# Performance work log

Hardware: AMD Instinct MI355X
Metric: run time of the kernel (lower is better)

The kernel has to match this reference:

```python
import jax, jax.numpy as jnp
import numpy as np

LOC_SIZE, CID_SIZE, UID_SIZE, TIM_SIZE = 10000, 300, 1000, 48
LOC_EMB, CID_EMB, UID_EMB, TIM_EMB = 256, 64, 64, 32
HID, ENC_HID = 500, 250            # hidden_size, history_hidden_size
SEQ, TGT = 2048, 256
INPUT = LOC_EMB + TIM_EMB + CID_EMB  # 352


def setup_inputs() -> dict:
    key = jax.random.key(0)
    ks = jax.random.split(key, 32)
    n = lambda i, shape, s=0.05: (jax.random.normal(ks[i], shape, dtype=jnp.float32) * s)
    d = {}
    d["loc"] = jax.random.randint(ks[0], (SEQ, 1), 0, LOC_SIZE)
    d["tim"] = jax.random.randint(ks[1], (SEQ, 1), 0, TIM_SIZE)
    d["cid"] = jax.random.randint(ks[2], (SEQ, 1), 0, CID_SIZE)
    d["uid"] = jax.random.randint(ks[3], (1,), 0, UID_SIZE)
    d["target"] = jax.random.randint(ks[4], (TGT, 1), 0, LOC_SIZE)
    d["target_len"] = TGT
    d["time_sim_matrix"] = jax.random.uniform(ks[5], (TIM_SIZE, TIM_SIZE), dtype=jnp.float32)
    # keep distances away from 0 since the model computes 1/dist
    d["poi_distance_matrix"] = jax.random.uniform(ks[6], (LOC_SIZE, LOC_SIZE), dtype=jnp.float32, minval=0.1, maxval=2.0)
    d["poi_cid_tim"] = jax.random.uniform(ks[7], (TIM_SIZE, CID_SIZE), dtype=jnp.float32)
    # embedding tables (emb_loc/emb_cid are pretrained+frozen in the original)
    d["weight"] = n(8, (LOC_SIZE, LOC_EMB))
    d["weight_cid"] = n(9, (CID_SIZE, CID_EMB))
    d["emb_uid_w"] = n(10, (UID_SIZE, UID_EMB))
    d["emb_tim_w"] = n(11, (TIM_SIZE, TIM_EMB))
    # bidirectional encoder LSTM (hidden 250), gate order i,f,g,o like torch
    d["enc_Wih_f"] = n(12, (4 * ENC_HID, INPUT))
    d["enc_Whh_f"] = n(13, (4 * ENC_HID, ENC_HID))
    d["enc_b_f"] = jnp.zeros((4 * ENC_HID,), jnp.float32)
    d["enc_Wih_b"] = n(14, (4 * ENC_HID, INPUT))
    d["enc_Whh_b"] = n(15, (4 * ENC_HID, ENC_HID))
    d["enc_b_b"] = jnp.zeros((4 * ENC_HID,), jnp.float32)
    # decoder LSTM (hidden 500)
    d["dec_Wih"] = n(16, (4 * HID, INPUT))
    d["dec_Whh"] = n(17, (4 * HID, HID))
    d["dec_b"] = jnp.zeros((4 * HID,), jnp.float32)
    # linear layers
    d["fc_user_w"] = n(18, (HID, UID_EMB))
    d["fc_user_b"] = jnp.zeros((HID,), jnp.float32)
    d["fc_final_w"] = n(19, (LOC_SIZE, 3 * HID))
    d["fc_final_b"] = jnp.zeros((LOC_SIZE,), jnp.float32)
    d["fc_final2_w"] = n(20, (HID, 3 * HID))
    d["fc_final2_b"] = jnp.zeros((HID,), jnp.float32)
    return d


def _lstm(x, Wih, Whh, b, H):
    """Single-layer LSTM, batch=1. x: [T, D] -> hs: [T, H]."""
    h0 = jnp.zeros((H,), x.dtype)
    c0 = jnp.zeros((H,), x.dtype)

    def step(carry, xt):
        h, c = carry
        z = Wih @ xt + Whh @ h + b
        i, f, g, o = jnp.split(z, 4)
        c = jax.nn.sigmoid(f) * c + jax.nn.sigmoid(i) * jnp.tanh(g)
        h = jax.nn.sigmoid(o) * jnp.tanh(c)
        return (h, c), h

    _, hs = jax.lax.scan(step, (h0, c0), x)
    return hs


def _table_attn(history, current, table, invert=False, causal=False):
    """Vectorized replacement for the nested-loop lookup attention.
    energies[i, j] = table[current[i], history[j]] (or its reciprocal),
    upper triangle left at 0 for the self-attn variants (as in the original),
    then softmax over the full row (torch F.softmax default dim=1 on 2D)."""
    e = table[current[:, None], history[None, :]]
    if invert:
        e = 1.0 / e
    if causal:
        nn_ = e.shape[0]
        e = jnp.where(jnp.tril(jnp.ones((nn_, nn_), bool)), e, jnp.zeros((), e.dtype))
    return jax.nn.softmax(e, axis=-1)


def reference(loc, tim, cid, uid, target, target_len,
              time_sim_matrix, poi_distance_matrix, poi_cid_tim,
              weight, weight_cid, emb_uid_w, emb_tim_w,
              enc_Wih_f, enc_Whh_f, enc_b_f, enc_Wih_b, enc_Whh_b, enc_b_b,
              dec_Wih, dec_Whh, dec_b,
              fc_user_w, fc_user_b, fc_final_w, fc_final_b, fc_final2_w, fc_final2_b):
    T = int(target_len)
    loc_f, tim_f, cid_f = loc[:, 0], tim[:, 0], cid[:, 0]

    # cross attention: current window attends to history via lookup tables
    attn_cid_time = _table_attn(cid_f[:-T], tim_f[-T:], poi_cid_tim)
    attn_loc = _table_attn(loc_f[:-T], loc_f[-T:], poi_distance_matrix, invert=True)
    attn_time = _table_attn(tim_f[:-T], tim_f[-T:], time_sim_matrix)
    # self attention on the current window (lower-triangular fill)
    self_cid_time = _table_attn(cid_f[-T:], tim_f[-T:], poi_cid_tim, causal=True)
    self_loc = _table_attn(loc_f[-T:], loc_f[-T:], poi_distance_matrix, invert=True, causal=True)
    self_time = _table_attn(tim_f[-T:], tim_f[-T:], time_sim_matrix, causal=True)

    # embeddings (dropout is identity in eval)
    x = jnp.concatenate([weight[loc_f], emb_tim_w[tim_f], weight_cid[cid_f]], axis=1)  # [SEQ, INPUT]
    hist_x, tgt_x = x[:-T], x[-T:]

    # bidirectional encoder over history
    hf = _lstm(hist_x, enc_Wih_f, enc_Whh_f, enc_b_f, ENC_HID)
    hb = _lstm(hist_x[::-1], enc_Wih_b, enc_Whh_b, enc_b_b, ENC_HID)[::-1]
    hidden_history = jnp.concatenate([hf, hb], axis=1)  # [SEQ-T, 2*ENC_HID=500]

    # decoder over current window
    hidden_state = _lstm(tgt_x, dec_Wih, dec_Whh, dec_b, HID)  # [T, 500]

    target_emb = weight[target[:, 0]]  # [T, LOC_EMB]

    uid_emb = emb_uid_w[uid] @ fc_user_w.T + fc_user_b  # [1, 500]
    user_attn = jax.nn.softmax(uid_emb @ hidden_history.T, axis=-1)  # [1, hist]
    context_user = user_attn @ hidden_history  # [1, 500]

    context = (attn_loc + attn_time + attn_cid_time) @ hidden_history  # [T, 500]
    hidden_state = (self_loc + self_time + self_cid_time) @ hidden_state  # [T, 500]

    hidden_state_all = hidden_state + uid_emb  # broadcast of repeat
    out = jnp.concatenate([hidden_state_all, context,
                           jnp.broadcast_to(context_user, (T, HID))], axis=1)  # [T, 1500]
    y = out @ fc_final_w.T + fc_final_b    # [T, LOC_SIZE]
    y1 = out @ fc_final2_w.T + fc_final2_b  # [T, HID]
    score = jax.nn.log_softmax(y, axis=-1)
    return score, y1, target_emb
```

## Files before the change

### kernel.cpp

```cpp
#include <hip/hip_runtime.h>
#include <stdint.h>

#define HIST 1792
#define TGT 256
#define SEQ 2048
#define INPUT 352
#define EHID 250
#define HID 500

typedef _Float16 h2_t __attribute__((ext_vector_type(2)));

static __device__ __forceinline__ float fdot2(uint32_t a, uint32_t b, float c) {
  return __builtin_amdgcn_fdot2(__builtin_bit_cast(h2_t, a),
                                __builtin_bit_cast(h2_t, b), c, false);
}
static __device__ __forceinline__ uint32_t packh2(float lo, float hi) {
  h2_t h; h[0] = (_Float16)lo; h[1] = (_Float16)hi;
  return __builtin_bit_cast(uint32_t, h);
}
static __device__ __forceinline__ uint4 packq(const float* p) {
  uint4 r;
  r.x = packh2(p[0], p[1]); r.y = packh2(p[2], p[3]);
  r.z = packh2(p[4], p[5]); r.w = packh2(p[6], p[7]);
  return r;
}
static __device__ __forceinline__ float dotq(uint4 w, uint4 h, float acc) {
  acc = fdot2(w.x, h.x, acc); acc = fdot2(w.y, h.y, acc);
  acc = fdot2(w.z, h.z, acc); acc = fdot2(w.w, h.w, acc);
  return acc;
}
static __device__ __forceinline__ float sigf(float x) {
  x = fminf(fmaxf(x, -30.f), 30.f);
  return 1.f / (1.f + __expf(-x));
}
static __device__ __forceinline__ float tanh_f(float x) {
  x = fminf(fmaxf(x, -15.f), 15.f);
  float e = __expf(2.f * x);
  return (e - 1.f) / (e + 1.f);
}
static __device__ __forceinline__ void spin_flag(volatile int* f) {
  while (__hip_atomic_load(f, __ATOMIC_ACQUIRE, __HIP_MEMORY_SCOPE_AGENT) == 0)
    __builtin_amdgcn_s_sleep(2);
}
static __device__ __forceinline__ void spin_cnt(volatile int* f, int target) {
  while (__hip_atomic_load(f, __ATOMIC_ACQUIRE, __HIP_MEMORY_SCOPE_AGENT) < target)
    __builtin_amdgcn_s_sleep(2);
}
#define AW(dst, src) asm("v_accvgpr_write_b32 %0, %1" : "=a"(dst) : "v"(src))
#define AR(dst, src) asm("v_accvgpr_read_b32 %0, %1" : "=v"(dst) : "a"(src))
#define ARQ(dst, arr, base) do { AR(dst.x, arr[(base)+0]); AR(dst.y, arr[(base)+1]); AR(dst.z, arr[(base)+2]); AR(dst.w, arr[(base)+3]); } while(0)

__global__ void k_gemm_t16(const float* __restrict__ A, int lda,
                           const float* __restrict__ W, int ldw,
                           const float* __restrict__ bias,
                           float* __restrict__ C, int ldc,
                           int M, int N, int K, int revA) {
  __shared__ uint32_t AsP[8][65];
  __shared__ uint32_t WsP[8][65];
  const int bn = blockIdx.x * 64, bm = blockIdx.y * 64;
  const int tid = threadIdx.x;
  const int tx = tid & 15, ty = tid >> 4;
  float acc[4][4] = {};
  for (int k0 = 0; k0 < K; k0 += 16) {
    for (int i = tid; i < 512; i += 256) {
      int m = i & 63, kk = i >> 6;
      int gm = bm + m, gk = k0 + 2 * kk;
      float v0 = 0.f, v1 = 0.f;
      if (gm < M) {
        int am = revA ? (M - 1 - gm) : gm;
        if (gk < K)     v0 = A[(size_t)am * lda + gk];
        if (gk + 1 < K) v1 = A[(size_t)am * lda + gk + 1];
      }
      AsP[kk][m] = packh2(v0, v1);
    }
    for (int i = tid; i < 512; i += 256) {
      int n = i & 63, kk = i >> 6;
      int gn = bn + n, gk = k0 + 2 * kk;
      float v0 = 0.f, v1 = 0.f;
      if (gn < N) {
        if (gk < K)     v0 = W[(size_t)gn * ldw + gk];
        if (gk + 1 < K) v1 = W[(size_t)gn * ldw + gk + 1];
      }
      WsP[kk][n] = packh2(v0, v1);
    }
    __syncthreads();
#pragma unroll
    for (int kk = 0; kk < 8; kk++) {
      uint32_t a0 = AsP[kk][ty * 4 + 0], a1 = AsP[kk][ty * 4 + 1], a2 = AsP[kk][ty * 4 + 2], a3 = AsP[kk][ty * 4 + 3];
      uint32_t b0 = WsP[kk][tx * 4 + 0], b1 = WsP[kk][tx * 4 + 1], b2 = WsP[kk][tx * 4 + 2], b3 = WsP[kk][tx * 4 + 3];
      acc[0][0] = fdot2(a0, b0, acc[0][0]); acc[0][1] = fdot2(a0, b1, acc[0][1]);
      acc[0][2] = fdot2(a0, b2, acc[0][2]); acc[0][3] = fdot2(a0, b3, acc[0][3]);
      acc[1][0] = fdot2(a1, b0, acc[1][0]); acc[1][1] = fdot2(a1, b1, acc[1][1]);
      acc[1][2] = fdot2(a1, b2, acc[1][2]); acc[1][3] = fdot2(a1, b3, acc[1][3]);
      acc[2][0] = fdot2(a2, b0, acc[2][0]); acc[2][1] = fdot2(a2, b1, acc[2][1]);
      acc[2][2] = fdot2(a2, b2, acc[2][2]); acc[2][3] = fdot2(a2, b3, acc[2][3]);
      acc[3][0] = fdot2(a3, b0, acc[3][0]); acc[3][1] = fdot2(a3, b1, acc[3][1]);
      acc[3][2] = fdot2(a3, b2, acc[3][2]); acc[3][3] = fdot2(a3, b3, acc[3][3]);
    }
    __syncthreads();
  }
  for (int i = 0; i < 4; i++) {
    int gm = bm + ty * 4 + i; if (gm >= M) continue;
    for (int j = 0; j < 4; j++) {
      int gn = bn + tx * 4 + j; if (gn >= N) continue;
      C[(size_t)gm * ldc + gn] = acc[i][j] + (bias ? bias[gn] : 0.f);
    }
  }
}

static __device__ void gemm_tile_emb(const int* __restrict__ loc, const int* __restrict__ tim,
                                     const int* __restrict__ cid,
                                     const float* __restrict__ weight,
                                     const float* __restrict__ emb_tim_w,
                                     const float* __restrict__ weight_cid,
                                     int rowoff,
                                     const float* __restrict__ W,
                                     const float* __restrict__ bias,
                                     float* __restrict__ C, int ldc,
                                     int M, int N, int bm, int bn, int revA,
                                     int tid, uint32_t* AsP, uint32_t* WsP) {
  const int tx = tid & 15, ty = (tid & 255) >> 4;
  float acc[4][4] = {};
  for (int k0 = 0; k0 < INPUT; k0 += 16) {
    {
      int m = tid & 63, kk = tid >> 6;
      int gm = bm + m, gk = k0 + 2 * kk;
      float v0 = 0.f, v1 = 0.f;
      if (gm < M) {
        int am = (revA ? (M - 1 - gm) : gm) + rowoff;
        if (gk < 256) {
          const float* wp = weight + (size_t)loc[am] * 256 + gk;
          v0 = wp[0]; v1 = wp[1];
        } else if (gk < 288) {
          const float* wp = emb_tim_w + tim[am] * 32 + (gk - 256);
          v0 = wp[0]; v1 = wp[1];
        } else {
          const float* wp = weight_cid + cid[am] * 64 + (gk - 288);
          v0 = wp[0]; v1 = wp[1];
        }
      }
      AsP[kk * 65 + m] = packh2(v0, v1);
      int gn = bn + m;
      float w0 = 0.f, w1 = 0.f;
      if (gn < N) {
        const float* wp = W + (size_t)gn * INPUT + gk;
        w0 = wp[0]; w1 = wp[1];
      }
      WsP[kk * 65 + m] = packh2(w0, w1);
    }
    __syncthreads();
    if (tid < 256) {
#pragma unroll
      for (int kk = 0; kk < 8; kk++) {
        uint32_t a0 = AsP[kk * 65 + ty * 4 + 0], a1 = AsP[kk * 65 + ty * 4 + 1];
        uint32_t a2 = AsP[kk * 65 + ty * 4 + 2], a3 = AsP[kk * 65 + ty * 4 + 3];
        uint32_t b0 = WsP[kk * 65 + tx * 4 + 0], b1 = WsP[kk * 65 + tx * 4 + 1];
        uint32_t b2 = WsP[kk * 65 + tx * 4 + 2], b3 = WsP[kk * 65 + tx * 4 + 3];
        acc[0][0] = fdot2(a0, b0, acc[0][0]); acc[0][1] = fdot2(a0, b1, acc[0][1]);
        acc[0][2] = fdot2(a0, b2, acc[0][2]); acc[0][3] = fdot2(a0, b3, acc[0][3]);
        acc[1][0] = fdot2(a1, b0, acc[1][0]); acc[1][1] = fdot2(a1, b1, acc[1][1]);
        acc[1][2] = fdot2(a1, b2, acc[1][2]); acc[1][3] = fdot2(a1, b3, acc[1][3]);
        acc[2][0] = fdot2(a2, b0, acc[2][0]); acc[2][1] = fdot2(a2, b1, acc[2][1]);
        acc[2][2] = fdot2(a2, b2, acc[2][2]); acc[2][3] = fdot2(a2, b3, acc[2][3]);
        acc[3][0] = fdot2(a3, b0, acc[3][0]); acc[3][1] = fdot2(a3, b1, acc[3][1]);
        acc[3][2] = fdot2(a3, b2, acc[3][2]); acc[3][3] = fdot2(a3, b3, acc[3][3]);
      }
    }
    __syncthreads();
  }
  if (tid < 256) {
    for (int i = 0; i < 4; i++) {
      int gm = bm + ty * 4 + i; if (gm >= M) continue;
      for (int j = 0; j < 4; j++) {
        int gn = bn + tx * 4 + j; if (gn >= N) continue;
        C[(size_t)gm * ldc + gn] = acc[i][j] + bias[gn];
      }
    }
  }
}

static __device__ void nn_tile_fused(const float* __restrict__ A, int lda,
                                     const float* __restrict__ B, int ldb,
                                     const float* __restrict__ addvec,
                                     float* __restrict__ C, int ldc,
                                     int M, int N, int K, int bm, int bn,
                                     int tid, uint32_t* AsP, uint32_t* BsP) {
  const int tx = tid & 15, ty = (tid & 255) >> 4;
  float acc[4][4] = {};
  for (int k0 = 0; k0 < K; k0 += 16) {
    {
      int m = tid & 63, kk = tid >> 6;
      int gm = bm + m, gk = k0 + 2 * kk;
      float v0 = 0.f, v1 = 0.f;
      if (gm < M) {
        if (gk < K)     v0 = A[(size_t)gm * lda + gk];
        if (gk + 1 < K) v1 = A[(size_t)gm * lda + gk + 1];
      }
      AsP[kk * 65 + m] = packh2(v0, v1);
      int gn = bn + m;
      float w0 = 0.f, w1 = 0.f;
      if (gn < N) {
        if (gk < K)     w0 = B[(size_t)gk * ldb + gn];
        if (gk + 1 < K) w1 = B[(size_t)(gk + 1) * ldb + gn];
      }
      BsP[kk * 65 + m] = packh2(w0, w1);
    }
    __syncthreads();
    if (tid < 256) {
#pragma unroll
      for (int kk = 0; kk < 8; kk++) {
        uint32_t a0 = AsP[kk * 65 + ty * 4 + 0], a1 = AsP[kk * 65 + ty * 4 + 1];
        uint32_t a2 = AsP[kk * 65 + ty * 4 + 2], a3 = AsP[kk * 65 + ty * 4 + 3];
        uint32_t b0 = BsP[kk * 65 + tx * 4 + 0], b1 = BsP[kk * 65 + tx * 4 + 1];
        uint32_t b2 = BsP[kk * 65 + tx * 4 + 2], b3 = BsP[kk * 65 + tx * 4 + 3];
        acc[0][0] = fdot2(a0, b0, acc[0][0]); acc[0][1] = fdot2(a0, b1, acc[0][1]);
        acc[0][2] = fdot2(a0, b2, acc[0][2]); acc[0][3] = fdot2(a0, b3, acc[0][3]);
        acc[1][0] = fdot2(a1, b0, acc[1][0]); acc[1][1] = fdot2(a1, b1, acc[1][1]);
        acc[1][2] = fdot2(a1, b2, acc[1][2]); acc[1][3] = fdot2(a1, b3, acc[1][3]);
        acc[2][0] = fdot2(a2, b0, acc[2][0]); acc[2][1] = fdot2(a2, b1, acc[2][1]);
        acc[2][2] = fdot2(a2, b2, acc[2][2]); acc[2][3] = fdot2(a2, b3, acc[2][3]);
        acc[3][0] = fdot2(a3, b0, acc[3][0]); acc[3][1] = fdot2(a3, b1, acc[3][1]);
        acc[3][2] = fdot2(a3, b2, acc[3][2]); acc[3][3] = fdot2(a3, b3, acc[3][3]);
      }
    }
    __syncthreads();
  }
  if (tid < 256) {
    for (int i = 0; i < 4; i++) {
      int gm = bm + ty * 4 + i; if (gm >= M) continue;
      for (int j = 0; j < 4; j++) {
        int gn = bn + tx * 4 + j; if (gn >= N) continue;
        C[(size_t)gm * ldc + gn] = acc[i][j] + (addvec ? addvec[gn] : 0.f);
      }
    }
  }
}

#define WQL 12
#define WBYTES (WQL * 512 * 16)
__launch_bounds__(512)
__global__ void k_lstm(float* __restrict__ A_f, float* __restrict__ A_b,
                       float* __restrict__ A_d,
                       const float* __restrict__ Wih_f, const float* __restrict__ b_f,
                       const float* __restrict__ Wih_b, const float* __restrict__ b_b,
                       const float* __restrict__ Wih_d, const float* __restrict__ b_d,
                       const float* __restrict__ Whh_f, const float* __restrict__ Whh_b,
                       const float* __restrict__ Whh_d,
                       float* __restrict__ hh, float* __restrict__ hdec,
                       float* zpub, uint32_t* hpub, int* flag_z, int* flag_h, int* cnt,
                       const int* __restrict__ loc, const int* __restrict__ tim,
                       const int* __restrict__ cid, const int* __restrict__ target,
                       const float* __restrict__ weight, const float* __restrict__ emb_tim_w,
                       const float* __restrict__ weight_cid,
                       const float* __restrict__ ts, const float* __restrict__ pd,
                       const float* __restrict__ pct,
                       float* __restrict__ S1, float* __restrict__ S2,
                       const int* __restrict__ uid, const float* __restrict__ emb_uid_w,
                       const float* __restrict__ fc_user_w, const float* __restrict__ fc_user_b,
                       float* __restrict__ uid_emb, float* __restrict__ te) {
  const int b = blockIdx.x;
  const int tid = threadIdx.x;
  __shared__ __align__(16) unsigned char smem[WBYTES + 2048 + 4096];
  uint4* wl = (uint4*)smem;
  uint4* hbuf = (uint4*)(smem + WBYTES);
  float* zbuf = (float*)(smem + WBYTES + 2048);

  if (b < 6 && tid < 128) hbuf[tid] = make_uint4(0, 0, 0, 0);

  if (b < 2) {
    float* A = (b == 0) ? A_f : A_b;
    const float* Whh = (b == 0) ? Whh_f : Whh_b;
    int* mycnt = cnt + b * 32;
    const bool act = tid < 500;
    uint4 wv0[10], wv1[10];
    uint32_t wa[128];
    if (act) {
      const float* wr0 = Whh + (size_t)tid * EHID;
      const float* wr1 = Whh + (size_t)(tid + 500) * EHID;
#pragma unroll
      for (int q = 0; q < 6; q++) {
        float t0[8], t1[8];
#pragma unroll
        for (int cc = 0; cc < 8; cc++) {
          int col = 208 + 8 * q + cc;
          t0[cc] = (col < EHID) ? wr0[col] : 0.f;
          t1[cc] = (col < EHID) ? wr1[col] : 0.f;
        }
        wl[(q * 2 + 0) * 512 + tid] = packq(t0);
        wl[(q * 2 + 1) * 512 + tid] = packq(t1);
      }
#pragma unroll
      for (int k = 0; k < 16; k++) {
        uint4 p0 = packq(wr0 + 8 * (10 + k));
        uint4 p1 = packq(wr1 + 8 * (10 + k));
        AW(wa[k * 4 + 0], p0.x); AW(wa[k * 4 + 1], p0.y);
        AW(wa[k * 4 + 2], p0.z); AW(wa[k * 4 + 3], p0.w);
        AW(wa[64 + k * 4 + 0], p1.x); AW(wa[64 + k * 4 + 1], p1.y);
        AW(wa[64 + k * 4 + 2], p1.z); AW(wa[64 + k * 4 + 3], p1.w);
      }
#pragma unroll
      for (int q = 0; q < 10; q++) { wv0[q] = packq(wr0 + 8 * q); wv1[q] = packq(wr1 + 8 * q); }
    }
    if (tid == 0) spin_cnt(&mycnt[0], 16);
    __syncthreads();
    float c = 0.f;
    float aA = act ? A[tid] : 0.f;
    float aB = act ? A[500 + tid] : 0.f;
    __syncthreads();
    for (int t = 0; t < HIST; t++) {
      const uint4* hb = hbuf + (t & 1) * 32;
      int tn = (t + 1 < HIST) ? t + 1 : t;
      if ((tn & 63) == 0 && tn > t) {
        if (tid == 0) spin_cnt(&mycnt[tn >> 6], 16);
        __syncthreads();
      }
      if (act) {
        float z0 = aA, z1 = aB, y0 = 0.f, y1 = 0.f;
        aA = A[tn * 1000 + tid];
        aB = A[tn * 1000 + 500 + tid];
#pragma unroll
        for (int q = 0; q < 10; q++) {
          uint4 hq = hb[q];
          z0 = dotq(wv0[q], hq, z0);
          z1 = dotq(wv1[q], hq, z1);
        }
#pragma unroll
        for (int k = 0; k < 16; k++) {
          uint4 hq = hb[10 + k];
          uint4 u0, u1;
          ARQ(u0, wa, k * 4);
          ARQ(u1, wa, 64 + k * 4);
          y0 = dotq(u0, hq, y0);
          y1 = dotq(u1, hq, y1);
        }
#pragma unroll
        for (int q = 0; q < 6; q++) {
          uint4 hq = hb[26 + q];
          z0 = dotq(wl[(q * 2 + 0) * 512 + tid], hq, z0);
          z1 = dotq(wl[(q * 2 + 1) * 512 + tid], hq, z1);
        }
        zbuf[tid] = z0 + y0;
        zbuf[500 + tid] = z1 + y1;
      }
      __syncthreads();
      float hval = 0.f;
      if (tid < EHID) {
        float zi = zbuf[tid], zf = zbuf[250 + tid], zg = zbuf[500 + tid], zo = zbuf[750 + tid];
        c = sigf(zf) * c + sigf(zi) * tanh_f(zg);
        hval = sigf(zo) * tanh_f(c);
        if (b == 0) hh[(size_t)t * HID + tid] = hval;
        else        hh[(size_t)(HIST - 1 - t) * HID + EHID + tid] = hval;
      }
      float hother = __shfl_xor(hval, 1);
      uint32_t* hw = (uint32_t*)(hbuf + ((t + 1) & 1) * 32);
      if (tid < EHID && !(tid & 1)) hw[tid >> 1] = packh2(hval, hother);
      __syncthreads();
    }
  } else if (b < 6) {
    const int gi = b - 2;
    const int j = tid;
    const bool act = (j < 500);
    int* dcnt = cnt + 64;
    uint4 wv[20];
    uint32_t wa[128];
    if (act) {
      const float* wr = Whh_d + (size_t)(gi * 500 + j) * HID;
#pragma unroll
      for (int q = 0; q < 12; q++) {
        float tmp[8];
#pragma unroll
        for (int cc = 0; cc < 8; cc++) {
          int col = 416 + 8 * q + cc;
          tmp[cc] = (col < HID) ? wr[col] : 0.f;
        }
        wl[q * 512 + tid] = packq(tmp);
      }
#pragma unroll
      for (int k = 0; k < 32; k++) {
        uint4 pq = packq(wr + 8 * (20 + k));
        AW(wa[k * 4 + 0], pq.x); AW(wa[k * 4 + 1], pq.y);
        AW(wa[k * 4 + 2], pq.z); AW(wa[k * 4 + 3], pq.w);
      }
#pragma unroll
      for (int q = 0; q < 20; q++) wv[q] = packq(wr + 8 * q);
    }
    if (tid == 0) spin_cnt(&dcnt[0], 32);
    __syncthreads();
    float c = 0.f;
    float aD = act ? A_d[gi * 500 + j] : 0.f;
    __syncthreads();
    for (int t = 0; t < TGT; t++) {
      const uint4* hb = hbuf + (t & 1) * 64;
      int tn = (t + 1 < TGT) ? t + 1 : t;
      if ((tn & 63) == 0 && tn > t) {
        if (tid == 0) spin_cnt(&dcnt[tn >> 6], 32);
        __syncthreads();
      }
      float z = 0.f;
      if (act) {
        float z0 = aD, z1 = 0.f, z2 = 0.f, z3 = 0.f;
        aD = A_d[tn * 2000 + gi * 500 + j];
#pragma unroll
        for (int q = 0; q < 20; q += 2) {
          z0 = dotq(wv[q], hb[q], z0);
          z1 = dotq(wv[q + 1], hb[q + 1], z1);
        }
#pragma unroll
        for (int k = 0; k < 32; k += 2) {
          uint4 u0, u1;
          ARQ(u0, wa, k * 4);
          ARQ(u1, wa, (k + 1) * 4);
          z2 = dotq(u0, hb[20 + k], z2);
          z3 = dotq(u1, hb[21 + k], z3);
        }
#pragma unroll
        for (int q = 0; q < 12; q += 2) {
          z0 = dotq(wl[q * 512 + tid], hb[52 + q], z0);
          z1 = dotq(wl[(q + 1) * 512 + tid], hb[53 + q], z1);
        }
        z = (z0 + z1) + (z2 + z3);
      }
      if (gi < 3) {
        if (act) zpub[gi * 512 + j] = z;
        __threadfence();
        __syncthreads();
        if (tid == 0) {
          __hip_atomic_store(&flag_z[t * 3 + gi], 1, __ATOMIC_RELEASE, __HIP_MEMORY_SCOPE_AGENT);
          spin_flag(&flag_h[t]);
        }
        __syncthreads();
        uint32_t* hw = (uint32_t*)(hbuf + ((t + 1) & 1) * 64);
        if (tid < 250)
          hw[tid] = __hip_atomic_load(&hpub[tid], __ATOMIC_RELAXED, __HIP_MEMORY_SCOPE_AGENT);
        __syncthreads();
      } else {
        if (tid == 0) {
          spin_flag(&flag_z[t * 3 + 0]);
          spin_flag(&flag_z[t * 3 + 1]);
          spin_flag(&flag_z[t * 3 + 2]);
        }
        __syncthreads();
        float hval = 0.f;
        if (act) {
          float zi = __hip_atomic_load(&zpub[0 * 512 + j], __ATOMIC_RELAXED, __HIP_MEMORY_SCOPE_AGENT);
          float zf = __hip_atomic_load(&zpub[1 * 512 + j], __ATOMIC_RELAXED, __HIP_MEMORY_SCOPE_AGENT);
          float zg = __hip_atomic_load(&zpub[2 * 512 + j], __ATOMIC_RELAXED, __HIP_MEMORY_SCOPE_AGENT);
          c = sigf(zf) * c + sigf(zi) * tanh_f(zg);
          hval = sigf(z) * tanh_f(c);
          hdec[(size_t)t * HID + j] = hval;
        }
        float hother = __shfl_xor(hval, 1);
        uint32_t* hw = (uint32_t*)(hbuf + ((t + 1) & 1) * 64);
        if (act && !(j & 1)) {
          uint32_t p = packh2(hval, hother);
          hw[j >> 1] = p;
          __hip_atomic_store(&hpub[j >> 1], p, __ATOMIC_RELAXED, __HIP_MEMORY_SCOPE_AGENT);
        }
        __threadfence();
        __syncthreads();
        if (tid == 0)
          __hip_atomic_store(&flag_h[t], 1, __ATOMIC_RELEASE, __HIP_MEMORY_SCOPE_AGENT);
      }
    }
  } else if (b == 6) {
    float* u = (float*)smem;
    if (tid < 64) u[tid] = emb_uid_w[(size_t)uid[0] * 64 + tid];
    __syncthreads();
    if (tid < HID) {
      float a = fc_user_b[tid];
      for (int k = 0; k < 64; k++) a += u[k] * fc_user_w[tid * 64 + k];
      uid_emb[tid] = a;
    }
  } else if (b < 903) {
    const int g = b - 7;
    const int chunk = g >> 5, w = g & 31;
    uint32_t* AsP = (uint32_t*)smem;
    uint32_t* WsP = AsP + 8 * 65;
    if (w < 16) {
      gemm_tile_emb(loc, tim, cid, weight, emb_tim_w, weight_cid, 0,
                    Wih_f, b_f, A_f, 1000, HIST, 1000, chunk * 64, w * 64, 0,
                    tid, AsP, WsP);
      __threadfence();
      __syncthreads();
      if (tid == 0)
        __hip_atomic_fetch_add(&cnt[chunk], 1, __ATOMIC_RELEASE, __HIP_MEMORY_SCOPE_AGENT);
    } else {
      gemm_tile_emb(loc, tim, cid, weight, emb_tim_w, weight_cid, 0,
                    Wih_b, b_b, A_b, 1000, HIST, 1000, chunk * 64, (w - 16) * 64, 1,
                    tid, AsP, WsP);
      __threadfence();
      __syncthreads();
      if (tid == 0)
        __hip_atomic_fetch_add(&cnt[32 + chunk], 1, __ATOMIC_RELEASE, __HIP_MEMORY_SCOPE_AGENT);
    }
  } else if (b < 1031) {
    const int g = b - 903;
    const int mt = g >> 5, nt = g & 31;
    uint32_t* AsP = (uint32_t*)smem;
    uint32_t* WsP = AsP + 8 * 65;
    gemm_tile_emb(loc, tim, cid, weight, emb_tim_w, weight_cid, HIST,
                  Wih_d, b_d, A_d, 2000, TGT, 2000, mt * 64, nt * 64, 0,
                  tid, AsP, WsP);
    __threadfence();
    __syncthreads();
    if (tid == 0)
      __hip_atomic_fetch_add(&cnt[64 + mt], 1, __ATOMIC_RELEASE, __HIP_MEMORY_SCOPE_AGENT);
  } else if (b < 1287) {
    const int i = b - 1031;
    float* e = (float*)smem;
    float* red = ((float*)smem) + HIST;
    const int loc_i = loc[HIST + i], tim_i = tim[HIST + i];
    for (int tab = 0; tab < 3; tab++) {
      for (int jj = tid; jj < HIST; jj += 512) {
        float v;
        if (tab == 0)      v = 1.f / pd[(size_t)loc_i * 10000 + loc[jj]];
        else if (tab == 1) v = ts[tim_i * 48 + tim[jj]];
        else               v = pct[tim_i * 300 + cid[jj]];
        e[jj] = v;
      }
      __syncthreads();
      float mx = -1e30f;
      for (int jj = tid; jj < HIST; jj += 512) mx = fmaxf(mx, e[jj]);
      red[tid] = mx; __syncthreads();
      for (int s = 256; s > 0; s >>= 1) { if (tid < s) red[tid] = fmaxf(red[tid], red[tid + s]); __syncthreads(); }
      mx = red[0]; __syncthreads();
      float sm = 0.f;
      for (int jj = tid; jj < HIST; jj += 512) sm += __expf(e[jj] - mx);
      red[tid] = sm; __syncthreads();
      for (int s = 256; s > 0; s >>= 1) { if (tid < s) red[tid] += red[tid + s]; __syncthreads(); }
      float inv = 1.f / red[0]; __syncthreads();
      for (int jj = tid; jj < HIST; jj += 512) {
        float p = __expf(e[jj] - mx) * inv;
        if (tab == 0) S1[(size_t)i * HIST + jj] = p; else S1[(size_t)i * HIST + jj] += p;
      }
      __syncthreads();
    }
    int lj = 0, tj = 0, cj = 0;
    if (tid < TGT) { lj = loc[HIST + tid]; tj = tim[HIST + tid]; cj = cid[HIST + tid]; }
    for (int tab = 0; tab < 3; tab++) {
      float v = 0.f;
      if (tid < TGT) {
        if (tab == 0)      v = 1.f / pd[(size_t)loc_i * 10000 + lj];
        else if (tab == 1) v = ts[tim_i * 48 + tj];
        else               v = pct[tim_i * 300 + cj];
        if (tid > i) v = 0.f;
        red[tid] = v;
      }
      __syncthreads();
      for (int s = 128; s > 0; s >>= 1) { if (tid < s) red[tid] = fmaxf(red[tid], red[tid + s]); __syncthreads(); }
      float mx = red[0]; __syncthreads();
      float ex = (tid < TGT) ? __expf(v - mx) : 0.f;
      if (tid < TGT) red[tid] = ex;
      __syncthreads();
      for (int s = 128; s > 0; s >>= 1) { if (tid < s) red[tid] += red[tid + s]; __syncthreads(); }
      float p = ex / red[0]; __syncthreads();
      if (tid < TGT) {
        if (tab == 0) S2[(size_t)i * TGT + tid] = p; else S2[(size_t)i * TGT + tid] += p;
      }
      __syncthreads();
    }
  } else {
    const int r0 = (b - 1287) * 16;
    for (int idx = tid; idx < 16 * 256; idx += 512) {
      int row = r0 + (idx >> 8), col = idx & 255;
      te[(size_t)row * 256 + col] = weight[(size_t)target[row] * 256 + col];
    }
  }
}

__launch_bounds__(512)
__global__ void k_tail(const float* __restrict__ uid_emb, const float* __restrict__ hh,
                       float* __restrict__ cu, int* cu_flag,
                       const float* __restrict__ Wf, const float* __restrict__ bf,
                       const float* __restrict__ W2, const float* __restrict__ b2,
                       float* __restrict__ fb, float* __restrict__ fb2,
                       const float* __restrict__ S2, const float* __restrict__ hdec,
                       const float* __restrict__ S1, float* __restrict__ outb) {
  const int b = blockIdx.x;
  const int tid = threadIdx.x;
  __shared__ __align__(16) float sh[HIST + 512];
  if (b == 0) {
    float* s = sh;
    float* red = sh + HIST;
    __shared__ __align__(16) float ue[HID];
    if (tid < HID) ue[tid] = uid_emb[tid];
    __syncthreads();
    for (int t = tid; t < HIST; t += 512) {
      const float4* hr = (const float4*)(hh + (size_t)t * HID);
      const float4* uv = (const float4*)ue;
      float a = 0.f;
#pragma unroll 5
      for (int k = 0; k < 125; k++) {
        float4 h4 = hr[k], u4 = uv[k];
        a += h4.x * u4.x + h4.y * u4.y + h4.z * u4.z + h4.w * u4.w;
      }
      s[t] = a;
    }
    __syncthreads();
    float mx = -1e30f;
    for (int t = tid; t < HIST; t += 512) mx = fmaxf(mx, s[t]);
    red[tid] = mx; __syncthreads();
    for (int st = 256; st > 0; st >>= 1) { if (tid < st) red[tid] = fmaxf(red[tid], red[tid + st]); __syncthreads(); }
    mx = red[0]; __syncthreads();
    float sm = 0.f;
    for (int t = tid; t < HIST; t += 512) sm += __expf(s[t] - mx);
    red[tid] = sm; __syncthreads();
    for (int st = 256; st > 0; st >>= 1) { if (tid < st) red[tid] += red[tid + st]; __syncthreads(); }
    float inv = 1.f / red[0]; __syncthreads();
    for (int t = tid; t < HIST; t += 512) s[t] = __expf(s[t] - mx) * inv;
    __syncthreads();
    if (tid < HID) {
      float a0 = 0.f, a1 = 0.f, a2 = 0.f, a3 = 0.f;
      for (int t = 0; t < HIST; t += 4) {
        a0 += s[t]     * hh[(size_t)t * HID + tid];
        a1 += s[t + 1] * hh[(size_t)(t + 1) * HID + tid];
        a2 += s[t + 2] * hh[(size_t)(t + 2) * HID + tid];
        a3 += s[t + 3] * hh[(size_t)(t + 3) * HID + tid];
      }
      cu[tid] = (a0 + a1) + (a2 + a3);
    }
    __threadfence();
    __syncthreads();
    if (tid == 0)
      __hip_atomic_store(cu_flag, 1, __ATOMIC_RELEASE, __HIP_MEMORY_SCOPE_AGENT);
  } else if (b < 22) {
    float* cus = sh;
    if (tid == 0) spin_flag(cu_flag);
    __syncthreads();
    if (tid < 500) cus[tid] = __hip_atomic_load(&cu[tid], __ATOMIC_RELAXED, __HIP_MEMORY_SCOPE_AGENT);
    __syncthreads();
    int n = (b - 1) * 512 + tid;
    const float4* cv = (const float4*)cus;
    if (n < 10000) {
      const float4* w = (const float4*)(Wf + (size_t)n * 1500 + 1000);
      float a = bf[n];
#pragma unroll 5
      for (int k = 0; k < 125; k++) {
        float4 wv = w[k], uv = cv[k];
        a += wv.x * uv.x + wv.y * uv.y + wv.z * uv.z + wv.w * uv.w;
      }
      fb[n] = a;
    } else if (n < 10500) {
      int m = n - 10000;
      const float4* w = (const float4*)(W2 + (size_t)m * 1500 + 1000);
      float a = b2[m];
#pragma unroll 5
      for (int k = 0; k < 125; k++) {
        float4 wv = w[k], uv = cv[k];
        a += wv.x * uv.x + wv.y * uv.y + wv.z * uv.z + wv.w * uv.w;
      }
      fb2[m] = a;
    }
  } else if (b < 54) {
    const int g = b - 22;
    const int nt = g & 7, mt = g >> 3;
    uint32_t* AsP = (uint32_t*)sh;
    uint32_t* BsP = AsP + 8 * 65;
    nn_tile_fused(S2, TGT, hdec, HID, uid_emb, outb, 1000,
                  TGT, HID, TGT, mt * 64, nt * 64, tid, AsP, BsP);
  } else {
    const int g = b - 54;
    const int nt = g & 7, mt = g >> 3;
    uint32_t* AsP = (uint32_t*)sh;
    uint32_t* BsP = AsP + 8 * 65;
    nn_tile_fused(S1, HIST, hh, HID, nullptr, outb + 500, 1000,
                  TGT, HID, HIST, mt * 64, nt * 64, tid, AsP, BsP);
  }
}

__global__ void k_logsoftmax(float* __restrict__ y) {
  const int i = blockIdx.x;
  const int tid = threadIdx.x;
  float* r = y + (size_t)i * 10000;
  __shared__ float red[1024];
  float mx = -1e30f;
  for (int j = tid; j < 10000; j += 1024) mx = fmaxf(mx, r[j]);
  red[tid] = mx; __syncthreads();
  for (int s = 512; s > 0; s >>= 1) { if (tid < s) red[tid] = fmaxf(red[tid], red[tid + s]); __syncthreads(); }
  mx = red[0]; __syncthreads();
  float sm = 0.f;
  for (int j = tid; j < 10000; j += 1024) sm += __expf(r[j] - mx);
  red[tid] = sm; __syncthreads();
  for (int s = 512; s > 0; s >>= 1) { if (tid < s) red[tid] += red[tid + s]; __syncthreads(); }
  float lse = mx + __logf(red[0]);
  __syncthreads();
  for (int j = tid; j < 10000; j += 1024) r[j] = r[j] - lse;
}

extern "C" void kernel_launch(void* const* d_in, const int* in_sizes, int n_in,
                              void* d_out, int out_size, void* d_ws, size_t ws_size,
                              hipStream_t stream) {
  (void)in_sizes; (void)n_in; (void)out_size; (void)ws_size;
  const int* loc = (const int*)d_in[0];
  const int* tim = (const int*)d_in[1];
  const int* cid = (const int*)d_in[2];
  const int* uid = (const int*)d_in[3];
  const int* target = (const int*)d_in[4];
  const float* ts = (const float*)d_in[6];
  const float* pd = (const float*)d_in[7];
  const float* pct = (const float*)d_in[8];
  const float* weight = (const float*)d_in[9];
  const float* weight_cid = (const float*)d_in[10];
  const float* emb_uid_w = (const float*)d_in[11];
  const float* emb_tim_w = (const float*)d_in[12];
  const float* enc_Wih_f = (const float*)d_in[13];
  const float* enc_Whh_f = (const float*)d_in[14];
  const float* enc_b_f = (const float*)d_in[15];
  const float* enc_Wih_b = (const float*)d_in[16];
  const float* enc_Whh_b = (const float*)d_in[17];
  const float* enc_b_b = (const float*)d_in[18];
  const float* dec_Wih = (const float*)d_in[19];
  const float* dec_Whh = (const float*)d_in[20];
  const float* dec_b = (const float*)d_in[21];
  const float* fc_user_w = (const float*)d_in[22];
  const float* fc_user_b = (const float*)d_in[23];
  const float* fc_final_w = (const float*)d_in[24];
  const float* fc_final_b = (const float*)d_in[25];
  const float* fc_final2_w = (const float*)d_in[26];
  const float* fc_final2_b = (const float*)d_in[27];

  float* score = (float*)d_out;
  float* y1 = score + (size_t)TGT * 10000;
  float* te = y1 + (size_t)TGT * HID;

  float* ws = (float*)d_ws;
  float* A_f = ws;
  float* A_b = A_f + (size_t)HIST * 1000;
  float* A_d = A_b + (size_t)HIST * 1000;
  float* hh = A_d + (size_t)TGT * 2000;
  float* hdec = hh + (size_t)HIST * HID;
  float* S1 = hdec + (size_t)TGT * HID;
  float* S2 = S1 + (size_t)TGT * HIST;
  float* outb = S2 + (size_t)TGT * TGT;
  float* cu = outb + (size_t)TGT * 1000;
  float* fb = cu + 512;
  float* fb2 = fb + 10016;
  float* uid_emb = fb2 + 512;
  float* zpub = uid_emb + 512;
  uint32_t* hpub = (uint32_t*)(zpub + 3 * 512);
  int* flag_z = (int*)(hpub + 256);
  int* flag_h = flag_z + 3 * TGT;
  int* cnt = flag_h + TGT;
  int* cu_flag = cnt + 96;
  const int n_flags = 4 * TGT + 96 + 1;

  hipMemsetAsync(flag_z, 0, n_flags * sizeof(int), stream);

  k_lstm<<<dim3(1303), dim3(512), 0, stream>>>(A_f, A_b, A_d,
                                               enc_Wih_f, enc_b_f, enc_Wih_b, enc_b_b,
                                               dec_Wih, dec_b,
                                               enc_Whh_f, enc_Whh_b, dec_Whh,
                                               hh, hdec, zpub, hpub, flag_z, flag_h, cnt,
                                               loc, tim, cid, target,
                                               weight, emb_tim_w, weight_cid,
                                               ts, pd, pct, S1, S2,
                                               uid, emb_uid_w, fc_user_w, fc_user_b,
                                               uid_emb, te);

  k_tail<<<dim3(86), dim3(512), 0, stream>>>(uid_emb, hh, cu, cu_flag,
                                             fc_final_w, fc_final_b,
                                             fc_final2_w, fc_final2_b, fb, fb2,
                                             S2, hdec, S1, outb);

  k_gemm_t16<<<dim3(157, 4), dim3(256), 0, stream>>>(outb, 1000, fc_final_w, 1500, fb, score, 10000, TGT, 10000, 1000, 0);
  k_gemm_t16<<<dim3(8, 4), dim3(256), 0, stream>>>(outb, 1000, fc_final2_w, 1500, fb2, y1, 500, TGT, 500, 1000, 0);

  k_logsoftmax<<<dim3(TGT), dim3(1024), 0, stream>>>(score);
}
```

Measured before the change: 4.647 ms.

## Fuse final GEMMs and log-softmax into tail kernel with counter-based dependencies

Merges the two output-projection GEMM launches and the log-softmax launch into the existing tail kernel. Blocks are ordered by dependency and wait on atomic counters for the bias, the attention-context row tiles and the score row tiles before starting. This is meant to remove kernel launch gaps and let independent tiles overlap across stages. In exchange, waiting blocks spin on their counters and can hold CU slots, and the GEMM tiles now run 512-thread blocks with only half the threads computing.

```diff
diff --git a/kernel.cpp b/kernel.cpp
--- a/kernel.cpp
+++ b/kernel.cpp
@@ -49,64 +49,6 @@
 #define AW(dst, src) asm("v_accvgpr_write_b32 %0, %1" : "=a"(dst) : "v"(src))
 #define AR(dst, src) asm("v_accvgpr_read_b32 %0, %1" : "=v"(dst) : "a"(src))
 #define ARQ(dst, arr, base) do { AR(dst.x, arr[(base)+0]); AR(dst.y, arr[(base)+1]); AR(dst.z, arr[(base)+2]); AR(dst.w, arr[(base)+3]); } while(0)
-
-__global__ void k_gemm_t16(const float* __restrict__ A, int lda,
-                           const float* __restrict__ W, int ldw,
-                           const float* __restrict__ bias,
-                           float* __restrict__ C, int ldc,
-                           int M, int N, int K, int revA) {
-  __shared__ uint32_t AsP[8][65];
-  __shared__ uint32_t WsP[8][65];
-  const int bn = blockIdx.x * 64, bm = blockIdx.y * 64;
-  const int tid = threadIdx.x;
-  const int tx = tid & 15, ty = tid >> 4;
-  float acc[4][4] = {};
-  for (int k0 = 0; k0 < K; k0 += 16) {
-    for (int i = tid; i < 512; i += 256) {
-      int m = i & 63, kk = i >> 6;
-      int gm = bm + m, gk = k0 + 2 * kk;
-      float v0 = 0.f, v1 = 0.f;
-      if (gm < M) {
-        int am = revA ? (M - 1 - gm) : gm;
-        if (gk < K)     v0 = A[(size_t)am * lda + gk];
-        if (gk + 1 < K) v1 = A[(size_t)am * lda + gk + 1];
-      }
-      AsP[kk][m] = packh2(v0, v1);
-    }
-    for (int i = tid; i < 512; i += 256) {
-      int n = i & 63, kk = i >> 6;
-      int gn = bn + n, gk = k0 + 2 * kk;
-      float v0 = 0.f, v1 = 0.f;
-      if (gn < N) {
-        if (gk < K)     v0 = W[(size_t)gn * ldw + gk];
-        if (gk + 1 < K) v1 = W[(size_t)gn * ldw + gk + 1];
-      }
-      WsP[kk][n] = packh2(v0, v1);
-    }
-    __syncthreads();
-#pragma unroll
-    for (int kk = 0; kk < 8; kk++) {
-      uint32_t a0 = AsP[kk][ty * 4 + 0], a1 = AsP[kk][ty * 4 + 1], a2 = AsP[kk][ty * 4 + 2], a3 = AsP[kk][ty * 4 + 3];
-      uint32_t b0 = WsP[kk][tx * 4 + 0], b1 = WsP[kk][tx * 4 + 1], b2 = WsP[kk][tx * 4 + 2], b3 = WsP[kk][tx * 4 + 3];
-      acc[0][0] = fdot2(a0, b0, acc[0][0]); acc[0][1] = fdot2(a0, b1, acc[0][1]);
-      acc[0][2] = fdot2(a0, b2, acc[0][2]); acc[0][3] = fdot2(a0, b3, acc[0][3]);
-      acc[1][0] = fdot2(a1, b0, acc[1][0]); acc[1][1] = fdot2(a1, b1, acc[1][1]);
-      acc[1][2] = fdot2(a1, b2, acc[1][2]); acc[1][3] = fdot2(a1, b3, acc[1][3]);
-      acc[2][0] = fdot2(a2, b0, acc[2][0]); acc[2][1] = fdot2(a2, b1, acc[2][1]);
-      acc[2][2] = fdot2(a2, b2, acc[2][2]); acc[2][3] = fdot2(a2, b3, acc[2][3]);
-      acc[3][0] = fdot2(a3, b0, acc[3][0]); acc[3][1] = fdot2(a3, b1, acc[3][1]);
-      acc[3][2] = fdot2(a3, b2, acc[3][2]); acc[3][3] = fdot2(a3, b3, acc[3][3]);
-    }
-    __syncthreads();
-  }
-  for (int i = 0; i < 4; i++) {
-    int gm = bm + ty * 4 + i; if (gm >= M) continue;
-    for (int j = 0; j < 4; j++) {
-      int gn = bn + tx * 4 + j; if (gn >= N) continue;
-      C[(size_t)gm * ldc + gn] = acc[i][j] + (bias ? bias[gn] : 0.f);
-    }
-  }
-}
 
 static __device__ void gemm_tile_emb(const int* __restrict__ loc, const int* __restrict__ tim,
                                      const int* __restrict__ cid,
@@ -236,6 +178,63 @@
   }
 }
 
+static __device__ void t_tile_fused(const float* __restrict__ A, int lda,
+                                    const float* __restrict__ W, int ldw,
+                                    const float* __restrict__ bias,
+                                    float* __restrict__ C, int ldc,
+                                    int M, int N, int K, int bm, int bn,
+                                    int tid, uint32_t* AsP, uint32_t* WsP) {
+  const int tx = tid & 15, ty = (tid & 255) >> 4;
+  float acc[4][4] = {};
+  for (int k0 = 0; k0 < K; k0 += 16) {
+    {
+      int m = tid & 63, kk = tid >> 6;
+      int gm = bm + m, gk = k0 + 2 * kk;
+      float v0 = 0.f, v1 = 0.f;
+      if (gm < M) {
+        if (gk < K)     v0 = A[(size_t)gm * lda + gk];
+        if (gk + 1 < K) v1 = A[(size_t)gm * lda + gk + 1];
+      }
+      AsP[kk * 65 + m] = packh2(v0, v1);
+      int gn = bn + m;
+      float w0 = 0.f, w1 = 0.f;
+      if (gn < N) {
+        if (gk < K)     w0 = W[(size_t)gn * ldw + gk];
+        if (gk + 1 < K) w1 = W[(size_t)gn * ldw + gk + 1];
+      }
+      WsP[kk * 65 + m] = packh2(w0, w1);
+    }
+    __syncthreads();
+    if (tid < 256) {
+#pragma unroll
+      for (int kk = 0; kk < 8; kk++) {
+        uint32_t a0 = AsP[kk * 65 + ty * 4 + 0], a1 = AsP[kk * 65 + ty * 4 + 1];
+        uint32_t a2 = AsP[kk * 65 + ty * 4 + 2], a3 = AsP[kk * 65 + ty * 4 + 3];
+        uint32_t b0 = WsP[kk * 65 + tx * 4 + 0], b1 = WsP[kk * 65 + tx * 4 + 1];
+        uint32_t b2 = WsP[kk * 65 + tx * 4 + 2], b3 = WsP[kk * 65 + tx * 4 + 3];
+        acc[0][0] = fdot2(a0, b0, acc[0][0]); acc[0][1] = fdot2(a0, b1, acc[0][1]);
+        acc[0][2] = fdot2(a0, b2, acc[0][2]); acc[0][3] = fdot2(a0, b3, acc[0][3]);
+        acc[1][0] = fdot2(a1, b0, acc[1][0]); acc[1][1] = fdot2(a1, b1, acc[1][1]);
+        acc[1][2] = fdot2(a1, b2, acc[1][2]); acc[1][3] = fdot2(a1, b3, acc[1][3]);
+        acc[2][0] = fdot2(a2, b0, acc[2][0]); acc[2][1] = fdot2(a2, b1, acc[2][1]);
+        acc[2][2] = fdot2(a2, b2, acc[2][2]); acc[2][3] = fdot2(a2, b3, acc[2][3]);
+        acc[3][0] = fdot2(a3, b0, acc[3][0]); acc[3][1] = fdot2(a3, b1, acc[3][1]);
+        acc[3][2] = fdot2(a3, b2, acc[3][2]); acc[3][3] = fdot2(a3, b3, acc[3][3]);
+      }
+    }
+    __syncthreads();
+  }
+  if (tid < 256) {
+    for (int i = 0; i < 4; i++) {
+      int gm = bm + ty * 4 + i; if (gm >= M) continue;
+      for (int j = 0; j < 4; j++) {
+        int gn = bn + tx * 4 + j; if (gn >= N) continue;
+        C[(size_t)gm * ldc + gn] = acc[i][j] + bias[gn];
+      }
+    }
+  }
+}
+
 #define WQL 12
 #define WBYTES (WQL * 512 * 16)
 __launch_bounds__(512)
@@ -570,12 +569,14 @@
 
 __launch_bounds__(512)
 __global__ void k_tail(const float* __restrict__ uid_emb, const float* __restrict__ hh,
-                       float* __restrict__ cu, int* cu_flag,
+                       float* __restrict__ cu, int* cu_flag, int* fbcnt,
+                       int* scnt, int* rcnt,
                        const float* __restrict__ Wf, const float* __restrict__ bf,
                        const float* __restrict__ W2, const float* __restrict__ b2,
                        float* __restrict__ fb, float* __restrict__ fb2,
                        const float* __restrict__ S2, const float* __restrict__ hdec,
-                       const float* __restrict__ S1, float* __restrict__ outb) {
+                       const float* __restrict__ S1, float* __restrict__ outb,
+                       float* __restrict__ score, float* __restrict__ y1) {
   const int b = blockIdx.x;
   const int tid = threadIdx.x;
   __shared__ __align__(16) float sh[HIST + 512];
@@ -651,6 +652,10 @@
       }
       fb2[m] = a;
     }
+    __threadfence();
+    __syncthreads();
+    if (tid == 0)
+      __hip_atomic_fetch_add(fbcnt, 1, __ATOMIC_RELEASE, __HIP_MEMORY_SCOPE_AGENT);
   } else if (b < 54) {
     const int g = b - 22;
     const int nt = g & 7, mt = g >> 3;
@@ -658,33 +663,62 @@
     uint32_t* BsP = AsP + 8 * 65;
     nn_tile_fused(S2, TGT, hdec, HID, uid_emb, outb, 1000,
                   TGT, HID, TGT, mt * 64, nt * 64, tid, AsP, BsP);
-  } else {
+    __threadfence();
+    __syncthreads();
+    if (tid == 0)
+      __hip_atomic_fetch_add(&scnt[mt], 1, __ATOMIC_RELEASE, __HIP_MEMORY_SCOPE_AGENT);
+  } else if (b < 86) {
     const int g = b - 54;
     const int nt = g & 7, mt = g >> 3;
     uint32_t* AsP = (uint32_t*)sh;
     uint32_t* BsP = AsP + 8 * 65;
     nn_tile_fused(S1, HIST, hh, HID, nullptr, outb + 500, 1000,
                   TGT, HID, HIST, mt * 64, nt * 64, tid, AsP, BsP);
+    __threadfence();
+    __syncthreads();
+    if (tid == 0)
+      __hip_atomic_fetch_add(&scnt[mt], 1, __ATOMIC_RELEASE, __HIP_MEMORY_SCOPE_AGENT);
+  } else if (b < 714) {
+    const int g = b - 86;
+    const int nt = g % 157, mt = g / 157;
+    if (tid == 0) { spin_cnt(fbcnt, 21); spin_cnt(&scnt[mt], 16); }
+    __syncthreads();
+    uint32_t* AsP = (uint32_t*)sh;
+    uint32_t* WsP = AsP + 8 * 65;
+    t_tile_fused(outb, 1000, Wf, 1500, fb, score, 10000,
+                 TGT, 10000, 1000, mt * 64, nt * 64, tid, AsP, WsP);
+    __threadfence();
+    __syncthreads();
+    if (tid == 0)
+      __hip_atomic_fetch_add(&rcnt[mt], 1, __ATOMIC_RELEASE, __HIP_MEMORY_SCOPE_AGENT);
+  } else if (b < 746) {
+    const int g = b - 714;
+    const int nt = g & 7, mt = g >> 3;
+    if (tid == 0) { spin_cnt(fbcnt, 21); spin_cnt(&scnt[mt], 16); }
+    __syncthreads();
+    uint32_t* AsP = (uint32_t*)sh;
+    uint32_t* WsP = AsP + 8 * 65;
+    t_tile_fused(outb, 1000, W2, 1500, fb2, y1, 500,
+                 TGT, 500, 1000, mt * 64, nt * 64, tid, AsP, WsP);
+  } else {
+    const int r = b - 746;
+    if (tid == 0) spin_cnt(&rcnt[r >> 6], 157);
+    __syncthreads();
+    float* red = sh;
+    float* row = score + (size_t)r * 10000;
+    float mx = -1e30f;
+    for (int j = tid; j < 10000; j += 512) mx = fmaxf(mx, row[j]);
+    red[tid] = mx; __syncthreads();
+    for (int s = 256; s > 0; s >>= 1) { if (tid < s) red[tid] = fmaxf(red[tid], red[tid + s]); __syncthreads(); }
+    mx = red[0]; __syncthreads();
+    float sm = 0.f;
+    for (int j = tid; j < 10000; j += 512) sm += __expf(row[j] - mx);
+    red[tid] = sm; __syncthreads();
+    for (int s = 256; s > 0; s >>= 1) { if (tid < s) red[tid] += red[tid + s]; __syncthreads(); }
+    float lse = mx + __logf(red[0]);
+    __syncthreads();
+    for (int j = tid; j < 10000; j += 512) row[j] = row[j] - lse;
   }
-}
-
-__global__ void k_logsoftmax(float* __restrict__ y) {
-  const int i = blockIdx.x;
-  const int tid = threadIdx.x;
-  float* r = y + (size_t)i * 10000;
-  __shared__ float red[1024];
-  float mx = -1e30f;
-  for (int j = tid; j < 10000; j += 1024) mx = fmaxf(mx, r[j]);
-  red[tid] = mx; __syncthreads();
-  for (int s = 512; s > 0; s >>= 1) { if (tid < s) red[tid] = fmaxf(red[tid], red[tid + s]); __syncthreads(); }
-  mx = red[0]; __syncthreads();
-  float sm = 0.f;
-  for (int j = tid; j < 10000; j += 1024) sm += __expf(r[j] - mx);
-  red[tid] = sm; __syncthreads();
-  for (int s = 512; s > 0; s >>= 1) { if (tid < s) red[tid] += red[tid + s]; __syncthreads(); }
-  float lse = mx + __logf(red[0]);
-  __syncthreads();
-  for (int j = tid; j < 10000; j += 1024) r[j] = r[j] - lse;
 }
 
 extern "C" void kernel_launch(void* const* d_in, const int* in_sizes, int n_in,
@@ -742,7 +776,10 @@
   int* flag_h = flag_z + 3 * TGT;
   int* cnt = flag_h + TGT;
   int* cu_flag = cnt + 96;
-  const int n_flags = 4 * TGT + 96 + 1;
+  int* fbcnt = cu_flag + 1;
+  int* scnt = fbcnt + 1;
+  int* rcnt = scnt + 4;
+  const int n_flags = 4 * TGT + 96 + 10;
 
   hipMemsetAsync(flag_z, 0, n_flags * sizeof(int), stream);
 
@@ -757,13 +794,8 @@
                                                uid, emb_uid_w, fc_user_w, fc_user_b,
                                                uid_emb, te);
 
-  k_tail<<<dim3(86), dim3(512), 0, stream>>>(uid_emb, hh, cu, cu_flag,
-                                             fc_final_w, fc_final_b,
-                                             fc_final2_w, fc_final2_b, fb, fb2,
-                                             S2, hdec, S1, outb);
-
-  k_gemm_t16<<<dim3(157, 4), dim3(256), 0, stream>>>(outb, 1000, fc_final_w, 1500, fb, score, 10000, TGT, 10000, 1000, 0);
-  k_gemm_t16<<<dim3(8, 4), dim3(256), 0, stream>>>(outb, 1000, fc_final2_w, 1500, fb2, y1, 500, TGT, 500, 1000, 0);
-
-  k_logsoftmax<<<dim3(TGT), dim3(1024), 0, stream>>>(score);
-}
+  k_tail<<<dim3(1002), dim3(512), 0, stream>>>(uid_emb, hh, cu, cu_flag, fbcnt, scnt, rcnt,
+                                               fc_final_w, fc_final_b,
+                                               fc_final2_w, fc_final2_b, fb, fb2,
+                                               S2, hdec, S1, outb, score, y1);
+}
```

New measurement: 6.084 ms. 30.9% more time.
